# Kernel tuning notes

Measured on AMD Instinct MI355X. Metric: run time of the kernel, lower is better.

## Reference

```python
import jax, jax.numpy as jnp
import numpy as np

MARGIN = 6.0
EPSILON = 2.0
REL_DIM = 256
REL_RANGE = (MARGIN + EPSILON) / REL_DIM  # OpenKE rel_embedding_range = 0.03125
PI = 3.14159265358979323846


def setup_inputs() -> dict:
    key = jax.random.key(0)
    k1, k2, k3, k4, k5 = jax.random.split(key, 5)
    B, S, H = 16, 64, 768
    E, D2 = 43234, 512  # entity count, entity embed dim (2*256)
    return {
        "question_hidden": jax.random.normal(k1, (B, S, H), dtype=jnp.float32),
        "W_rel": jax.random.normal(k2, (18, H), dtype=jnp.float32) * 0.02,
        "b_rel": jnp.zeros((18,), dtype=jnp.float32),
        "rel_embeddings": jax.random.normal(k3, (18, REL_DIM), dtype=jnp.float32) * REL_RANGE,
        "ent_embeddings": jax.random.normal(k4, (E, D2), dtype=jnp.float32) * 0.05,
        "head_id": jax.random.randint(k5, (B,), 0, E, dtype=jnp.int64),
    }


def reference(question_hidden, W_rel, b_rel, rel_embeddings, ent_embeddings, head_id):
    # RelationPredictor: mean-pool BERT hidden states, then Linear(768 -> 18)
    q = jnp.mean(question_hidden, axis=1)                       # (B, 768)
    rel_scores = q @ W_rel.T + b_rel                            # (B, 18)
    # soft relation mixture -> predicted relation embedding
    predict_relation = jax.nn.sigmoid(rel_scores) @ rel_embeddings  # (B, 256)
    head = ent_embeddings[head_id]                              # (B, 512)
    re_h, im_h = jnp.split(head, 2, axis=-1)                    # (B, 256) each
    phase = predict_relation / (REL_RANGE / PI)
    re_r, im_r = jnp.cos(phase), jnp.sin(phase)
    # rotate head by relation (complex multiply)
    rot_re = re_h * re_r - im_h * im_r                          # (B, 256)
    rot_im = re_h * im_r + im_h * re_r                          # (B, 256)
    re_t, im_t = jnp.split(ent_embeddings, 2, axis=-1)          # (E, 256) each
    # broadcast distance vs all entities: (B, E, 256) intermediates
    dre = rot_re[:, None, :] - re_t[None, :, :]
    dim_ = rot_im[:, None, :] - im_t[None, :, :]
    dist = jnp.sqrt(dre * dre + dim_ * dim_).sum(axis=-1)       # (B, E)
    return MARGIN - dist
```

## Files before the change

kernel.cpp:

```cpp
#include <hip/hip_runtime.h>
#include <hip/hip_bf16.h>
#include <math.h>

#define MARGIN_F 6.0f
#define PHASE_SCALE 100.53096491487338f

__global__ void k_prep(const float* __restrict__ qh, const float* __restrict__ W,
                       const float* __restrict__ brel,
                       const float* __restrict__ rel,
                       const float* __restrict__ ent, const int* __restrict__ hid,
                       float* __restrict__ rot) {
    __shared__ float q[768];
    __shared__ float sig[18];
    int b = blockIdx.x;
    int t = threadIdx.x;

    if (t < 768) {
        float s = 0.f;
        const float* base = qh + (size_t)b * 64 * 768 + t;
        #pragma unroll 8
        for (int srow = 0; srow < 64; ++srow) s += base[(size_t)srow * 768];
        q[t] = s * (1.0f / 64.0f);
    }
    __syncthreads();

    int wave = t >> 6, lane = t & 63;
    for (int r = wave; r < 18; r += 16) {
        float p = 0.f;
        for (int h = lane; h < 768; h += 64) p += q[h] * W[r * 768 + h];
        for (int off = 32; off; off >>= 1) p += __shfl_xor(p, off, 64);
        if (lane == 0) sig[r] = 1.0f / (1.0f + expf(-(p + brel[r])));
    }
    __syncthreads();

    if (t < 256) {
        int d = t;
        float pr = 0.f;
        #pragma unroll
        for (int r = 0; r < 18; ++r) pr += sig[r] * rel[r * 256 + d];
        float phase = pr * PHASE_SCALE;
        float sn, cs;
        sincosf(phase, &sn, &cs);
        int h0 = hid[b];
        float reh = ent[(size_t)h0 * 512 + d];
        float imh = ent[(size_t)h0 * 512 + 256 + d];
        rot[b * 256 + d]        = reh * cs - imh * sn;
        rot[4096 + b * 256 + d] = reh * sn + imh * cs;
    }
}

__global__ __launch_bounds__(256, 4) void k_dist(const float* __restrict__ ent,
                                                 const float* __restrict__ rot,
                                                 float* __restrict__ out, int E,
                                                 int chunk) {
    int lane = threadIdx.x & 63;
    int wid = blockIdx.x * 4 + (threadIdx.x >> 6);
    int bhalf = wid & 1;
    int pair = wid >> 1;

    const float4* rre4 = (const float4*)rot + (size_t)bhalf * 8 * 64;
    const float4* rim4 = (const float4*)(rot + 4096) + (size_t)bhalf * 8 * 64;
    float4 rre[8], rim[8];
    #pragma unroll
    for (int b = 0; b < 8; ++b) {
        rre[b] = rre4[b * 64 + lane];
        rim[b] = rim4[b * 64 + lane];
    }

    int bout = bhalf * 8 + ((lane & 1) << 2) | (lane & 2) | ((lane >> 2) & 1);
    bout = bhalf * 8 + (((lane & 1) << 2) | (lane & 2) | ((lane >> 2) & 1));

    int e0 = (int)((long long)pair * chunk);
    int e1 = min(e0 + chunk, E);
    if (e0 >= e1) return;

    const float4* r4 = (const float4*)(ent + (size_t)e0 * 512);
    float4 te = r4[lane];
    float4 ti = r4[64 + lane];

    for (int e = e0; e < e1; ++e) {
        float4 nte = make_float4(0.f, 0.f, 0.f, 0.f);
        float4 nti = nte;
        if (e + 1 < e1) {
            const float4* n4 = (const float4*)(ent + (size_t)(e + 1) * 512);
            nte = n4[lane];
            nti = n4[64 + lane];
        }

        float v[8];
        #pragma unroll
        for (int b = 0; b < 8; ++b) {
            float dx0 = rre[b].x - te.x, dy0 = rim[b].x - ti.x;
            float dx1 = rre[b].y - te.y, dy1 = rim[b].y - ti.y;
            float dx2 = rre[b].z - te.z, dy2 = rim[b].z - ti.z;
            float dx3 = rre[b].w - te.w, dy3 = rim[b].w - ti.w;
            float s0 = __builtin_amdgcn_sqrtf(dx0 * dx0 + dy0 * dy0);
            float s1 = __builtin_amdgcn_sqrtf(dx1 * dx1 + dy1 * dy1);
            float s2 = __builtin_amdgcn_sqrtf(dx2 * dx2 + dy2 * dy2);
            float s3 = __builtin_amdgcn_sqrtf(dx3 * dx3 + dy3 * dy3);
            v[b] = (s0 + s1) + (s2 + s3);
        }

        #pragma unroll
        for (int i = 0; i < 4; ++i) {
            float send = (lane & 1) ? v[i] : v[i + 4];
            float recv = __shfl_xor(send, 1, 64);
            v[i] = ((lane & 1) ? v[i + 4] : v[i]) + recv;
        }
        #pragma unroll
        for (int i = 0; i < 2; ++i) {
            float send = (lane & 2) ? v[i] : v[i + 2];
            float recv = __shfl_xor(send, 2, 64);
            v[i] = ((lane & 2) ? v[i + 2] : v[i]) + recv;
        }
        {
            float send = (lane & 4) ? v[0] : v[1];
            float recv = __shfl_xor(send, 4, 64);
            v[0] = ((lane & 4) ? v[1] : v[0]) + recv;
        }
        v[0] += __shfl_xor(v[0], 8, 64);
        v[0] += __shfl_xor(v[0], 16, 64);
        v[0] += __shfl_xor(v[0], 32, 64);

        if (lane < 8) out[(size_t)bout * E + e] = MARGIN_F - v[0];

        te = nte;
        ti = nti;
    }
}

extern "C" void kernel_launch(void* const* d_in, const int* in_sizes, int n_in,
                              void* d_out, int out_size, void* d_ws,
                              size_t ws_size, hipStream_t stream) {
    const float* qh   = (const float*)d_in[0];
    const float* W    = (const float*)d_in[1];
    const float* brel = (const float*)d_in[2];
    const float* rel  = (const float*)d_in[3];
    const float* ent  = (const float*)d_in[4];
    const int*   hid  = (const int*)d_in[5];
    float* out = (float*)d_out;

    int E = in_sizes[4] / 512;

    float* rot = (float*)d_ws;

    k_prep<<<dim3(16), 1024, 0, stream>>>(qh, W, brel, rel, ent, hid, rot);

    const int NB = 1024;
    int npairs = NB * 4 / 2;
    int chunk = (E + npairs - 1) / npairs;
    k_dist<<<dim3(NB), 256, 0, stream>>>(ent, rot, out, E, chunk);
}
```

Measured before the change: 63.18 us.

## Reload rotated head vectors per entity to cut registers and raise occupancy

Removes the 64 register-resident float4 rotated-head values and the software prefetch of the next entity row, instead reloading rot vectors from global memory (L1-cached) inside the loop. Launch bounds rise to 8 blocks per CU and the grid doubles to 2048 blocks, so each wave covers fewer entities. The aim is to trade register pressure for occupancy to hide memory latency, at the cost of 16 extra vector loads per entity iteration and losing explicit prefetch.

```diff
diff --git a/kernel.cpp b/kernel.cpp
--- a/kernel.cpp
+++ b/kernel.cpp
@@ -49,7 +49,7 @@
     }
 }
 
-__global__ __launch_bounds__(256, 4) void k_dist(const float* __restrict__ ent,
+__global__ __launch_bounds__(256, 8) void k_dist(const float* __restrict__ ent,
                                                  const float* __restrict__ rot,
                                                  float* __restrict__ out, int E,
                                                  int chunk) {
@@ -60,40 +60,27 @@
 
     const float4* rre4 = (const float4*)rot + (size_t)bhalf * 8 * 64;
     const float4* rim4 = (const float4*)(rot + 4096) + (size_t)bhalf * 8 * 64;
-    float4 rre[8], rim[8];
-    #pragma unroll
-    for (int b = 0; b < 8; ++b) {
-        rre[b] = rre4[b * 64 + lane];
-        rim[b] = rim4[b * 64 + lane];
-    }
 
-    int bout = bhalf * 8 + ((lane & 1) << 2) | (lane & 2) | ((lane >> 2) & 1);
-    bout = bhalf * 8 + (((lane & 1) << 2) | (lane & 2) | ((lane >> 2) & 1));
+    int bout = bhalf * 8 + (((lane & 1) << 2) | (lane & 2) | ((lane >> 2) & 1));
 
     int e0 = (int)((long long)pair * chunk);
     int e1 = min(e0 + chunk, E);
     if (e0 >= e1) return;
 
-    const float4* r4 = (const float4*)(ent + (size_t)e0 * 512);
-    float4 te = r4[lane];
-    float4 ti = r4[64 + lane];
-
     for (int e = e0; e < e1; ++e) {
-        float4 nte = make_float4(0.f, 0.f, 0.f, 0.f);
-        float4 nti = nte;
-        if (e + 1 < e1) {
-            const float4* n4 = (const float4*)(ent + (size_t)(e + 1) * 512);
-            nte = n4[lane];
-            nti = n4[64 + lane];
-        }
+        const float4* r4 = (const float4*)(ent + (size_t)e * 512);
+        float4 te = r4[lane];
+        float4 ti = r4[64 + lane];
 
         float v[8];
         #pragma unroll
         for (int b = 0; b < 8; ++b) {
-            float dx0 = rre[b].x - te.x, dy0 = rim[b].x - ti.x;
-            float dx1 = rre[b].y - te.y, dy1 = rim[b].y - ti.y;
-            float dx2 = rre[b].z - te.z, dy2 = rim[b].z - ti.z;
-            float dx3 = rre[b].w - te.w, dy3 = rim[b].w - ti.w;
+            float4 rr = rre4[b * 64 + lane];
+            float4 ri = rim4[b * 64 + lane];
+            float dx0 = rr.x - te.x, dy0 = ri.x - ti.x;
+            float dx1 = rr.y - te.y, dy1 = ri.y - ti.y;
+            float dx2 = rr.z - te.z, dy2 = ri.z - ti.z;
+            float dx3 = rr.w - te.w, dy3 = ri.w - ti.w;
             float s0 = __builtin_amdgcn_sqrtf(dx0 * dx0 + dy0 * dy0);
             float s1 = __builtin_amdgcn_sqrtf(dx1 * dx1 + dy1 * dy1);
             float s2 = __builtin_amdgcn_sqrtf(dx2 * dx2 + dy2 * dy2);
@@ -123,9 +110,6 @@
         v[0] += __shfl_xor(v[0], 32, 64);
 
         if (lane < 8) out[(size_t)bout * E + e] = MARGIN_F - v[0];
-
-        te = nte;
-        ti = nti;
     }
 }
 
@@ -146,7 +130,7 @@
 
     k_prep<<<dim3(16), 1024, 0, stream>>>(qh, W, brel, rel, ent, hid, rot);
 
-    const int NB = 1024;
+    const int NB = 2048;
     int npairs = NB * 4 / 2;
     int chunk = (E + npairs - 1) / npairs;
     k_dist<<<dim3(NB), 256, 0, stream>>>(ent, rot, out, E, chunk);
```

New measurement: 148.6 us. +135.3%, slower.
